# Kernel tuning notes

Hardware: AMD Instinct MI355X
Metric: run time of the kernel (lower is better)

## Reference

```python
import jax, jax.numpy as jnp
import numpy as np

N_EMBD = 1024
N_HEAD = 16
B, T = 4, 2048

def setup_inputs() -> dict:
    key = jax.random.key(0)
    k1, k2, k3 = jax.random.split(key, 3)
    scale = 0.02
    return {
        "x": jax.random.normal(k1, (B, T, N_EMBD), dtype=jnp.float32),
        "W_qkv": jax.random.normal(k2, (N_EMBD, 3 * N_EMBD), dtype=jnp.float32) * scale,
        "b_qkv": jnp.zeros((3 * N_EMBD,), dtype=jnp.float32),
        "W_proj": jax.random.normal(k3, (N_EMBD, N_EMBD), dtype=jnp.float32) * scale,
        "b_proj": jnp.zeros((N_EMBD,), dtype=jnp.float32),
    }

def reference(x, W_qkv, b_qkv, W_proj, b_proj):
    Bb, Tt, C = x.shape
    hs = C // N_HEAD  # head_size
    qkv = x @ W_qkv + b_qkv                      # [B,T,3C]
    q, k, v = jnp.split(qkv, 3, axis=-1)
    # [B,T,C] -> [B,H,T,hs]
    def to_heads(t):
        return t.reshape(Bb, Tt, N_HEAD, hs).transpose(0, 2, 1, 3)
    q, k, v = to_heads(q), to_heads(k), to_heads(v)
    scores = jnp.einsum('bhqd,bhkd->bhqk', q, k) * (1.0 / np.sqrt(hs))
    causal = jnp.tril(jnp.ones((Tt, Tt), dtype=bool))
    scores = jnp.where(causal, scores, -jnp.inf)
    weights = jax.nn.softmax(scores, axis=-1)    # dropout=0.0 -> identity
    out = jnp.einsum('bhqk,bhkd->bhqd', weights, v)
    out = out.transpose(0, 2, 1, 3).reshape(Bb, Tt, C)
    return out @ W_proj + b_proj
```

## Files before the change

### kernel.cpp

```cpp
#include <hip/hip_runtime.h>
#include <cstdint>

typedef _Float16 f16;
typedef _Float16 f16x4 __attribute__((ext_vector_type(4)));
typedef _Float16 f16x8 __attribute__((ext_vector_type(8)));
typedef float f32x4 __attribute__((ext_vector_type(4)));

constexpr int NB = 4, NT = 2048, NC = 1024, NH = 16, HS = 64;
constexpr int Mtot = NB * NT;
constexpr int BM = 128, BN = 128;

__device__ __forceinline__ void gll16(const f16* g, f16* l) {
  __builtin_amdgcn_global_load_lds(
      (const __attribute__((address_space(1))) unsigned int*)(uintptr_t)g,
      (__attribute__((address_space(3))) unsigned int*)(uintptr_t)l, 16, 0, 0);
}

__global__ __launch_bounds__(256) void prep(
    const float* __restrict__ X, const float* __restrict__ Wq,
    const float* __restrict__ Wp,
    f16* __restrict__ Xh, f16* __restrict__ Wqt, f16* __restrict__ Wpt)
{
  const int bx = blockIdx.x;
  const int t = threadIdx.x;
  if (bx < 4096) {
    const size_t i = ((size_t)bx * 256 + t) * 8;
    float4 a = *reinterpret_cast<const float4*>(X + i);
    float4 b = *reinterpret_cast<const float4*>(X + i + 4);
    f16x8 o;
    o[0] = (f16)a.x; o[1] = (f16)a.y; o[2] = (f16)a.z; o[3] = (f16)a.w;
    o[4] = (f16)b.x; o[5] = (f16)b.y; o[6] = (f16)b.z; o[7] = (f16)b.w;
    *reinterpret_cast<f16x8*>(Xh + i) = o;
    return;
  }
  __shared__ __align__(16) f16 Ts[64 * 72];
  const int t2 = bx - 4096;
  const int nt = t2 & 63;
  const int k0 = (t2 >> 6) * 64;
  const float* src; f16* dst; int Ndim, n0;
  if (nt < 48) { src = Wq; dst = Wqt; Ndim = 3 * NC; n0 = nt * 64; }
  else         { src = Wp; dst = Wpt; Ndim = NC;     n0 = (nt - 48) * 64; }
  const int kl = t >> 2, nb = (t & 3) * 16;
#pragma unroll
  for (int i = 0; i < 4; ++i) {
    float4 vv = *reinterpret_cast<const float4*>(
        src + (size_t)(k0 + kl) * Ndim + n0 + nb + 4 * i);
    f16x4 h; h[0] = (f16)vv.x; h[1] = (f16)vv.y; h[2] = (f16)vv.z; h[3] = (f16)vv.w;
    *reinterpret_cast<f16x4*>(&Ts[kl * 72 + nb + 4 * i]) = h;
  }
  __syncthreads();
  const int nl = t >> 2, kb = (t & 3) * 16;
#pragma unroll
  for (int i = 0; i < 2; ++i) {
    f16x8 o;
#pragma unroll
    for (int j = 0; j < 8; ++j) o[j] = Ts[(kb + 8 * i + j) * 72 + nl];
    *reinterpret_cast<f16x8*>(dst + (size_t)(n0 + nl) * NC + k0 + kb + 8 * i) = o;
  }
}

template <int MODE>
__global__ __launch_bounds__(256) void gemm_f16(
    const f16* __restrict__ A, const f16* __restrict__ Bt,
    const float* __restrict__ bias,
    f16* __restrict__ Qh, f16* __restrict__ Kh, f16* __restrict__ Vh,
    float* __restrict__ Out, int ntiles)
{
  __shared__ __align__(16) f16 As[BM * 64];
  __shared__ __align__(16) f16 Bs[BN * 64];
  const int tid = threadIdx.x;
  const int flat = blockIdx.x;
  const int cpx = gridDim.x >> 3;
  const int v = (flat & 7) * cpx + (flat >> 3);
  const int m0 = (v / ntiles) * BM;
  const int n0 = (v % ntiles) * BN;
  const int w = tid >> 6, l = tid & 63;
  const int wr = w >> 1, wc = w & 1;
  const int lr = l & 15, hi = l >> 4;

  f32x4 acc[4][4];
#pragma unroll
  for (int i = 0; i < 4; ++i)
#pragma unroll
    for (int j = 0; j < 4; ++j) acc[i][j] = (f32x4){0.f, 0.f, 0.f, 0.f};

  const int lrow = l >> 3;
  const int lsrc = ((l & 7) ^ lrow) * 8;

  for (int k0 = 0; k0 < NC; k0 += 64) {
    __syncthreads();
#pragma unroll
    for (int i = 0; i < 4; ++i) {
      const int rr = 32 * w + 8 * i;
      gll16(A  + (size_t)(m0 + rr + lrow) * NC + k0 + lsrc, &As[rr * 64]);
      gll16(Bt + (size_t)(n0 + rr + lrow) * NC + k0 + lsrc, &Bs[rr * 64]);
    }
    __syncthreads();
#pragma unroll
    for (int kk = 0; kk < 2; ++kk) {
      f16x8 a[4], b[4];
#pragma unroll
      for (int mi = 0; mi < 4; ++mi) {
        int row = wr * 64 + mi * 16 + lr;
        int idx = (row * 64 + kk * 32 + hi * 8) ^ ((row & 7) << 3);
        a[mi] = *reinterpret_cast<const f16x8*>(&As[idx]);
      }
#pragma unroll
      for (int ni = 0; ni < 4; ++ni) {
        int row = wc * 64 + ni * 16 + lr;
        int idx = (row * 64 + kk * 32 + hi * 8) ^ ((row & 7) << 3);
        b[ni] = *reinterpret_cast<const f16x8*>(&Bs[idx]);
      }
#pragma unroll
      for (int mi = 0; mi < 4; ++mi)
#pragma unroll
        for (int ni = 0; ni < 4; ++ni)
          acc[mi][ni] = __builtin_amdgcn_mfma_f32_16x16x32_f16(
              a[mi], b[ni], acc[mi][ni], 0, 0, 0);
    }
  }

  if (MODE == 0) {
#pragma unroll
    for (int ni = 0; ni < 4; ++ni) {
      int colg = n0 + wc * 64 + ni * 16 + lr;
      int which = colg >> 10;
      int c = colg & (NC - 1);
      int h = c >> 6, d = c & 63;
      float bv = bias[colg];
      if (which == 2) {
#pragma unroll
        for (int mi = 0; mi < 4; ++mi) {
          int rowg = m0 + wr * 64 + mi * 16 + hi * 4;
          int b = rowg >> 11, tt = rowg & (NT - 1);
          int slot = ((tt >> 5) & 1) * 32 + ((tt >> 2) & 3) * 8 + ((tt >> 4) & 1) * 4;
          f16x4 pk;
#pragma unroll
          for (int r = 0; r < 4; ++r) pk[r] = (f16)(acc[mi][ni][r] + bv);
          *reinterpret_cast<f16x4*>(
              &Vh[(size_t)(b * NH + h) * NT * HS + (tt >> 6) * 4096 + d * 64 + slot]) = pk;
        }
      } else {
        f16* dst = (which == 0) ? Qh : Kh;
#pragma unroll
        for (int mi = 0; mi < 4; ++mi) {
#pragma unroll
          for (int r = 0; r < 4; ++r) {
            int rowg = m0 + wr * 64 + mi * 16 + hi * 4 + r;
            int b = rowg >> 11, t = rowg & (NT - 1);
            dst[(((size_t)(b * NH + h) * NT) + t) * HS + d] =
                (f16)(acc[mi][ni][r] + bv);
          }
        }
      }
    }
  } else {
#pragma unroll
    for (int ni = 0; ni < 4; ++ni) {
      int colg = n0 + wc * 64 + ni * 16 + lr;
      float bv = bias[colg];
#pragma unroll
      for (int mi = 0; mi < 4; ++mi) {
#pragma unroll
        for (int r = 0; r < 4; ++r) {
          int rowg = m0 + wr * 64 + mi * 16 + hi * 4 + r;
          Out[(size_t)rowg * NC + colg] = acc[mi][ni][r] + bv;
        }
      }
    }
  }
}

__global__ __launch_bounds__(128, 2) void flash_attn(
    const f16* __restrict__ Qh, const f16* __restrict__ Kh,
    const f16* __restrict__ Vh, f16* __restrict__ att)
{
  __shared__ __align__(16) f16 Ks[2][64 * 64];
  __shared__ __align__(16) f16 Vt[2][64 * 64];

  const int tid = threadIdx.x;
  const int w = tid >> 6, l = tid & 63;
  const int lr = l & 15, g = l >> 4;

  const int flat = blockIdx.x;
  const int v = (flat & 7) * 128 + (flat >> 3);
  const int pairi = v & 15;
  const int bh = v >> 4;

  const f16* Qb = Qh + (size_t)bh * NT * HS;
  const f16* Kb = Kh + (size_t)bh * NT * HS;
  const f16* Vb = Vh + (size_t)bh * NT * HS;
  const int ob = bh >> 4, oh = bh & (NH - 1);

  const int srow = tid >> 1;
  const int scol = (tid & 1) * 32;
  const int vs = ((srow + (srow >> 3)) & 7) << 3;

  f16x8 kpre[4], vpre[4];
#pragma unroll
  for (int ii = 0; ii < 4; ++ii) {
    kpre[ii] = *reinterpret_cast<const f16x8*>(Kb + (size_t)srow * HS + scol + 8 * ii);
    vpre[ii] = *reinterpret_cast<const f16x8*>(Vb + (size_t)srow * HS + scol + 8 * ii);
  }

  for (int seg = 0; seg < 2; ++seg) {
    const int qt = (seg == 0) ? pairi : 31 - pairi;
    const int qbase = qt * 64 + w * 32;
    const int jtmax = qt;

    f16x8 qB[2][2];
#pragma unroll
    for (int mt = 0; mt < 2; ++mt)
#pragma unroll
      for (int ds = 0; ds < 2; ++ds) {
        f16x8 t = *reinterpret_cast<const f16x8*>(
            Qb + (size_t)(qbase + 16 * mt + lr) * HS + 32 * ds + 8 * g);
#pragma unroll
        for (int j = 0; j < 8; ++j) t[j] = t[j] * (f16)0.18033688f;
        qB[mt][ds] = t;
      }

    f32x4 Ot[2][4];
    float m_run[2], l_run[2];
#pragma unroll
    for (int mt = 0; mt < 2; ++mt) {
#pragma unroll
      for (int dt = 0; dt < 4; ++dt) Ot[mt][dt] = (f32x4){0.f, 0.f, 0.f, 0.f};
      m_run[mt] = -INFINITY; l_run[mt] = 0.f;
    }

    for (int jt = 0; jt <= jtmax; ++jt) {
      const int cur = jt & 1;
#pragma unroll
      for (int ii = 0; ii < 4; ++ii) {
        int c0 = scol + 8 * ii;
        *reinterpret_cast<f16x8*>(&Ks[cur][srow * 64 + (c0 ^ ((srow & 7) << 3))]) = kpre[ii];
        *reinterpret_cast<f16x8*>(&Vt[cur][srow * 64 + (c0 ^ vs)]) = vpre[ii];
      }
      const bool more = (jt < jtmax) || (seg == 0);
      if (more) {
        const int nj = (jt < jtmax) ? jt + 1 : 0;
#pragma unroll
        for (int ii = 0; ii < 4; ++ii) {
          kpre[ii] = *reinterpret_cast<const f16x8*>(
              Kb + (size_t)(nj * 64 + srow) * HS + scol + 8 * ii);
          vpre[ii] = *reinterpret_cast<const f16x8*>(
              Vb + (size_t)(nj * 64 + srow) * HS + scol + 8 * ii);
        }
      }
      __syncthreads();

      const bool needMask = (jt * 64 + 63) > qbase;

      f16x8 aK[4][2];
#pragma unroll
      for (int kt2 = 0; kt2 < 4; ++kt2) {
        int row = 16 * kt2 + lr;
#pragma unroll
        for (int ds = 0; ds < 2; ++ds)
          aK[kt2][ds] = *reinterpret_cast<const f16x8*>(
              &Ks[cur][row * 64 + ((32 * ds + 8 * g) ^ ((row & 7) << 3))]);
      }

      f32x4 St[2][4];
#pragma unroll
      for (int mt = 0; mt < 2; ++mt)
#pragma unroll
        for (int kt2 = 0; kt2 < 4; ++kt2) St[mt][kt2] = (f32x4){0.f, 0.f, 0.f, 0.f};
      __builtin_amdgcn_s_setprio(1);
#pragma unroll
      for (int mt = 0; mt < 2; ++mt)
#pragma unroll
        for (int kt2 = 0; kt2 < 4; ++kt2)
#pragma unroll
          for (int ds = 0; ds < 2; ++ds)
            St[mt][kt2] = __builtin_amdgcn_mfma_f32_16x16x32_f16(
                aK[kt2][ds], qB[mt][ds], St[mt][kt2], 0, 0, 0);
      __builtin_amdgcn_s_setprio(0);

      if (needMask) {
#pragma unroll
        for (int mt = 0; mt < 2; ++mt) {
          const int qg = qbase + 16 * mt + lr;
#pragma unroll
          for (int kt2 = 0; kt2 < 4; ++kt2)
#pragma unroll
            for (int r = 0; r < 4; ++r)
              if ((jt * 64 + 16 * kt2 + 4 * g + r) > qg) St[mt][kt2][r] = -INFINITY;
        }
      }

      float pm0 = -INFINITY, pm1 = -INFINITY;
#pragma unroll
      for (int kt2 = 0; kt2 < 4; ++kt2)
#pragma unroll
        for (int r = 0; r < 4; ++r) {
          pm0 = fmaxf(pm0, St[0][kt2][r]);
          pm1 = fmaxf(pm1, St[1][kt2][r]);
        }
      {
        float a0 = __shfl_xor(pm0, 16), a1 = __shfl_xor(pm1, 16);
        pm0 = fmaxf(pm0, a0); pm1 = fmaxf(pm1, a1);
        a0 = __shfl_xor(pm0, 32); a1 = __shfl_xor(pm1, 32);
        pm0 = fmaxf(pm0, a0); pm1 = fmaxf(pm1, a1);
      }
      float mo0 = m_run[0], mo1 = m_run[1];
      const bool need0 = !__all(pm0 <= mo0 + 8.0f);
      const bool need1 = !__all(pm1 <= mo1 + 8.0f);
      if (need0) {
        float mn = fmaxf(mo0, pm0);
        float al = exp2f(mo0 - mn);
        l_run[0] *= al;
#pragma unroll
        for (int dt = 0; dt < 4; ++dt)
#pragma unroll
          for (int r = 0; r < 4; ++r) Ot[0][dt][r] *= al;
        m_run[0] = mn; mo0 = mn;
      }
      if (need1) {
        float mn = fmaxf(mo1, pm1);
        float al = exp2f(mo1 - mn);
        l_run[1] *= al;
#pragma unroll
        for (int dt = 0; dt < 4; ++dt)
#pragma unroll
          for (int r = 0; r < 4; ++r) Ot[1][dt][r] *= al;
        m_run[1] = mn; mo1 = mn;
      }
      f16x8 pB[2][2];
      float ts0 = 0.f, ts1 = 0.f;
#pragma unroll
      for (int kt2 = 0; kt2 < 4; ++kt2)
#pragma unroll
        for (int r = 0; r < 4; ++r) {
          float p0 = exp2f(St[0][kt2][r] - mo0);
          float p1 = exp2f(St[1][kt2][r] - mo1);
          ts0 += p0; ts1 += p1;
          pB[0][kt2 >> 1][(kt2 & 1) * 4 + r] = (f16)p0;
          pB[1][kt2 >> 1][(kt2 & 1) * 4 + r] = (f16)p1;
        }
      {
        float a0 = __shfl_xor(ts0, 16), a1 = __shfl_xor(ts1, 16);
        ts0 += a0; ts1 += a1;
        a0 = __shfl_xor(ts0, 32); a1 = __shfl_xor(ts1, 32);
        ts0 += a0; ts1 += a1;
      }
      l_run[0] += ts0;
      l_run[1] += ts1;

      __builtin_amdgcn_s_setprio(1);
#pragma unroll
      for (int kt = 0; kt < 2; ++kt)
#pragma unroll
        for (int dt = 0; dt < 4; ++dt) {
          int d = 16 * dt + lr;
          int s = (d + (d >> 3)) & 7;
          f16x8 vA = *reinterpret_cast<const f16x8*>(
              &Vt[cur][d * 64 + ((32 * kt + 8 * g) ^ (s << 3))]);
#pragma unroll
          for (int mt = 0; mt < 2; ++mt)
            Ot[mt][dt] = __builtin_amdgcn_mfma_f32_16x16x32_f16(
                vA, pB[mt][kt], Ot[mt][dt], 0, 0, 0);
        }
      __builtin_amdgcn_s_setprio(0);
    }

    __syncthreads();
    f16* scr = &Ks[0][0] + w * 2048;
#pragma unroll
    for (int mt = 0; mt < 2; ++mt) {
      float inv = 1.f / l_run[mt];
      int q = 16 * mt + lr;
#pragma unroll
      for (int dt = 0; dt < 4; ++dt) {
        f16x4 ok;
#pragma unroll
        for (int r = 0; r < 4; ++r) ok[r] = (f16)(Ot[mt][dt][r] * inv);
        *reinterpret_cast<f16x4*>(
            &scr[q * 64 + ((16 * dt + 4 * g) ^ ((q & 7) << 3))]) = ok;
      }
    }
    const int orow = l >> 1;
    const int ocol = (l & 1) * 32;
#pragma unroll
    for (int i = 0; i < 4; ++i) {
      f16x8 ov = *reinterpret_cast<const f16x8*>(
          &scr[orow * 64 + ((ocol + i * 8) ^ ((orow & 7) << 3))]);
      *reinterpret_cast<f16x8*>(
          &att[((size_t)(ob * NT + qbase + orow)) * NC + oh * HS + ocol + i * 8]) = ov;
    }
    __syncthreads();
  }
}

extern "C" void kernel_launch(void* const* d_in, const int* in_sizes, int n_in,
                              void* d_out, int out_size, void* d_ws, size_t ws_size,
                              hipStream_t stream)
{
  (void)in_sizes; (void)n_in; (void)out_size; (void)ws_size;
  const float* x     = (const float*)d_in[0];
  const float* Wqkv  = (const float*)d_in[1];
  const float* bqkv  = (const float*)d_in[2];
  const float* Wproj = (const float*)d_in[3];
  const float* bproj = (const float*)d_in[4];
  float* out = (float*)d_out;

  const size_t HE = (size_t)NB * NH * NT * HS;
  f16* Qh  = (f16*)d_ws;
  f16* Kh  = Qh + HE;
  f16* Vh  = Kh + HE;
  f16* XA  = Vh + HE;
  f16* Wqt = XA + HE;
  f16* Wpt = Wqt + (size_t)3 * NC * NC;

  prep<<<dim3(4096 + 1024), 256, 0, stream>>>(x, Wqkv, Wproj, XA, Wqt, Wpt);
  gemm_f16<0><<<dim3(64 * 24), 256, 0, stream>>>(XA, Wqt, bqkv, Qh, Kh, Vh, nullptr, 24);
  flash_attn<<<dim3(1024), 128, 0, stream>>>(Qh, Kh, Vh, XA);
  gemm_f16<1><<<dim3(64 * 8), 256, 0, stream>>>(XA, Wpt, bproj, nullptr, nullptr, nullptr, out, 8);
}
```

Before: 181.8 us.

## Process both causal query tiles in one KV sweep with direct-to-LDS loads

The attention kernel now handles its two paired query tiles (pairi and 31-pairi) together in a single pass over K/V tiles, instead of making two sequential sweeps. This lets the shared K/V tiles in LDS serve both query tiles, removing the repeated loads for the shorter segment. K/V staging also moves from register prefetch plus LDS stores to global_load_lds into a double buffer, with the swizzle applied on the source address. In exchange, each thread holds two sets of accumulators and Q fragments, which raises register pressure and may lower occupancy. The second epilogue also writes through the scratch area without a barrier between the two epilogue calls, which could be a hazard.

After: 185.9 us. +2.3%, slower.

```diff
diff --git a/kernel.cpp b/kernel.cpp
--- a/kernel.cpp
+++ b/kernel.cpp
@@ -192,76 +192,83 @@
   const f16* Vb = Vh + (size_t)bh * NT * HS;
   const int ob = bh >> 4, oh = bh & (NH - 1);
 
-  const int srow = tid >> 1;
-  const int scol = (tid & 1) * 32;
-  const int vs = ((srow + (srow >> 3)) & 7) << 3;
-
-  f16x8 kpre[4], vpre[4];
-#pragma unroll
-  for (int ii = 0; ii < 4; ++ii) {
-    kpre[ii] = *reinterpret_cast<const f16x8*>(Kb + (size_t)srow * HS + scol + 8 * ii);
-    vpre[ii] = *reinterpret_cast<const f16x8*>(Vb + (size_t)srow * HS + scol + 8 * ii);
-  }
-
-  for (int seg = 0; seg < 2; ++seg) {
-    const int qt = (seg == 0) ? pairi : 31 - pairi;
-    const int qbase = qt * 64 + w * 32;
-    const int jtmax = qt;
-
-    f16x8 qB[2][2];
-#pragma unroll
-    for (int mt = 0; mt < 2; ++mt)
-#pragma unroll
-      for (int ds = 0; ds < 2; ++ds) {
-        f16x8 t = *reinterpret_cast<const f16x8*>(
-            Qb + (size_t)(qbase + 16 * mt + lr) * HS + 32 * ds + 8 * g);
-#pragma unroll
-        for (int j = 0; j < 8; ++j) t[j] = t[j] * (f16)0.18033688f;
-        qB[mt][ds] = t;
-      }
-
-    f32x4 Ot[2][4];
-    float m_run[2], l_run[2];
-#pragma unroll
-    for (int mt = 0; mt < 2; ++mt) {
-#pragma unroll
-      for (int dt = 0; dt < 4; ++dt) Ot[mt][dt] = (f32x4){0.f, 0.f, 0.f, 0.f};
-      m_run[mt] = -INFINITY; l_run[mt] = 0.f;
-    }
-
-    for (int jt = 0; jt <= jtmax; ++jt) {
-      const int cur = jt & 1;
-#pragma unroll
-      for (int ii = 0; ii < 4; ++ii) {
-        int c0 = scol + 8 * ii;
-        *reinterpret_cast<f16x8*>(&Ks[cur][srow * 64 + (c0 ^ ((srow & 7) << 3))]) = kpre[ii];
-        *reinterpret_cast<f16x8*>(&Vt[cur][srow * 64 + (c0 ^ vs)]) = vpre[ii];
-      }
-      const bool more = (jt < jtmax) || (seg == 0);
-      if (more) {
-        const int nj = (jt < jtmax) ? jt + 1 : 0;
-#pragma unroll
-        for (int ii = 0; ii < 4; ++ii) {
-          kpre[ii] = *reinterpret_cast<const f16x8*>(
-              Kb + (size_t)(nj * 64 + srow) * HS + scol + 8 * ii);
-          vpre[ii] = *reinterpret_cast<const f16x8*>(
-              Vb + (size_t)(nj * 64 + srow) * HS + scol + 8 * ii);
-        }
-      }
-      __syncthreads();
-
+  const int qt0 = pairi, qt1 = 31 - pairi;
+  const int qb0 = qt0 * 64 + w * 32;
+  const int qb1 = qt1 * 64 + w * 32;
+
+  const int lrow = l >> 3;
+  const int lsrc = ((l & 7) ^ lrow) * 8;
+
+#pragma unroll
+  for (int i = 0; i < 4; ++i) {
+    const int rr = 32 * w + 8 * i;
+    const int row = rr + lrow;
+    gll16(Kb + (size_t)row * HS + lsrc, &Ks[0][rr * 64]);
+    gll16(Vb + (size_t)row * 64 + (((l & 7) ^ ((row + (row >> 3)) & 7)) * 8),
+          &Vt[0][rr * 64]);
+  }
+
+  f16x8 qB0[2][2], qB1[2][2];
+#pragma unroll
+  for (int mt = 0; mt < 2; ++mt)
+#pragma unroll
+    for (int ds = 0; ds < 2; ++ds) {
+      f16x8 t0 = *reinterpret_cast<const f16x8*>(
+          Qb + (size_t)(qb0 + 16 * mt + lr) * HS + 32 * ds + 8 * g);
+      f16x8 t1 = *reinterpret_cast<const f16x8*>(
+          Qb + (size_t)(qb1 + 16 * mt + lr) * HS + 32 * ds + 8 * g);
+#pragma unroll
+      for (int j = 0; j < 8; ++j) {
+        t0[j] = t0[j] * (f16)0.18033688f;
+        t1[j] = t1[j] * (f16)0.18033688f;
+      }
+      qB0[mt][ds] = t0; qB1[mt][ds] = t1;
+    }
+
+  f32x4 Ot0[2][4], Ot1[2][4];
+  float m_run0[2], l_run0[2], m_run1[2], l_run1[2];
+#pragma unroll
+  for (int mt = 0; mt < 2; ++mt) {
+#pragma unroll
+    for (int dt = 0; dt < 4; ++dt) {
+      Ot0[mt][dt] = (f32x4){0.f, 0.f, 0.f, 0.f};
+      Ot1[mt][dt] = (f32x4){0.f, 0.f, 0.f, 0.f};
+    }
+    m_run0[mt] = -INFINITY; l_run0[mt] = 0.f;
+    m_run1[mt] = -INFINITY; l_run1[mt] = 0.f;
+  }
+
+  for (int jt = 0; jt <= qt1; ++jt) {
+    const int cur = jt & 1;
+    __syncthreads();
+
+    if (jt < qt1) {
+      const int nj = jt + 1;
+#pragma unroll
+      for (int i = 0; i < 4; ++i) {
+        const int rr = 32 * w + 8 * i;
+        const int row = rr + lrow;
+        gll16(Kb + (size_t)(nj * 64 + row) * HS + lsrc, &Ks[cur ^ 1][rr * 64]);
+        gll16(Vb + (size_t)nj * 4096 + (size_t)row * 64 +
+                  (((l & 7) ^ ((row + (row >> 3)) & 7)) * 8),
+              &Vt[cur ^ 1][rr * 64]);
+      }
+    }
+
+    f16x8 aK[4][2];
+#pragma unroll
+    for (int kt2 = 0; kt2 < 4; ++kt2) {
+      int row = 16 * kt2 + lr;
+#pragma unroll
+      for (int ds = 0; ds < 2; ++ds)
+        aK[kt2][ds] = *reinterpret_cast<const f16x8*>(
+            &Ks[cur][row * 64 + ((32 * ds + 8 * g) ^ ((row & 7) << 3))]);
+    }
+
+    auto seg_compute = [&](int qbase, const f16x8 (&qB)[2][2],
+                           f32x4 (&Ot)[2][4], float (&m_run)[2],
+                           float (&l_run)[2]) {
       const bool needMask = (jt * 64 + 63) > qbase;
-
-      f16x8 aK[4][2];
-#pragma unroll
-      for (int kt2 = 0; kt2 < 4; ++kt2) {
-        int row = 16 * kt2 + lr;
-#pragma unroll
-        for (int ds = 0; ds < 2; ++ds)
-          aK[kt2][ds] = *reinterpret_cast<const f16x8*>(
-              &Ks[cur][row * 64 + ((32 * ds + 8 * g) ^ ((row & 7) << 3))]);
-      }
-
       f32x4 St[2][4];
 #pragma unroll
       for (int mt = 0; mt < 2; ++mt)
@@ -363,10 +370,17 @@
                 vA, pB[mt][kt], Ot[mt][dt], 0, 0, 0);
         }
       __builtin_amdgcn_s_setprio(0);
-    }
-
-    __syncthreads();
-    f16* scr = &Ks[0][0] + w * 2048;
+    };
+
+    seg_compute(qb1, qB1, Ot1, m_run1, l_run1);
+    if (jt <= qt0)
+      seg_compute(qb0, qB0, Ot0, m_run0, l_run0);
+  }
+
+  __syncthreads();
+  f16* scr = &Ks[0][0] + w * 2048;
+
+  auto epilogue = [&](int qbase, f32x4 (&Ot)[2][4], float (&l_run)[2]) {
 #pragma unroll
     for (int mt = 0; mt < 2; ++mt) {
       float inv = 1.f / l_run[mt];
@@ -389,8 +403,10 @@
       *reinterpret_cast<f16x8*>(
           &att[((size_t)(ob * NT + qbase + orow)) * NC + oh * HS + ocol + i * 8]) = ov;
     }
-    __syncthreads();
-  }
+  };
+
+  epilogue(qb0, Ot0, l_run0);
+  epilogue(qb1, Ot1, l_run1);
 }
 
 extern "C" void kernel_launch(void* const* d_in, const int* in_sizes, int n_in,
```
